# Kernel optimization log

Hardware: AMD Instinct MI355X
Metric: run time of the kernel (lower is better)

Reference implementation:

```python
import jax, jax.numpy as jnp
import numpy as np

B, S, D, H, DFF = 4, 2048, 1024, 16, 4096
DK = D // H
EPS = 1e-5


def _linear_params(key, fan_in, fan_out):
    kw, kb = jax.random.split(key)
    bound = 1.0 / np.sqrt(fan_in)
    w = jax.random.uniform(kw, (fan_in, fan_out), minval=-bound, maxval=bound, dtype=jnp.float32)
    b = jax.random.uniform(kb, (fan_out,), minval=-bound, maxval=bound, dtype=jnp.float32)
    return w, b


def setup_inputs() -> dict:
    key = jax.random.key(0)
    ks = jax.random.split(key, 8)
    x = jax.random.normal(ks[0], (B, S, D), dtype=jnp.float32)
    mask = jnp.ones((B, 1, 1, S), dtype=jnp.int32)
    wq, bq = _linear_params(ks[1], D, D)
    wk, bk = _linear_params(ks[2], D, D)
    wv, bv = _linear_params(ks[3], D, D)
    wo, bo = _linear_params(ks[4], D, D)
    w1, b1 = _linear_params(ks[5], D, DFF)
    w2, b2 = _linear_params(ks[6], DFF, D)
    g1 = jnp.ones((D,), jnp.float32); be1 = jnp.zeros((D,), jnp.float32)
    g2 = jnp.ones((D,), jnp.float32); be2 = jnp.zeros((D,), jnp.float32)
    return {"x": x, "mask": mask, "wq": wq, "bq": bq, "wk": wk, "bk": bk,
            "wv": wv, "bv": bv, "wo": wo, "bo": bo, "w1": w1, "b1": b1,
            "w2": w2, "b2": b2, "g1": g1, "be1": be1, "g2": g2, "be2": be2}


def _layernorm(x, g, b):
    mu = jnp.mean(x, axis=-1, keepdims=True)
    var = jnp.mean(jnp.square(x - mu), axis=-1, keepdims=True)
    return (x - mu) * jax.lax.rsqrt(var + EPS) * g + b


def reference(x, mask, wq, bq, wk, bk, wv, bv, wo, bo, w1, b1, w2, b2, g1, be1, g2, be2):
    # Multi-head self-attention
    q = (x @ wq + bq).reshape(B, S, H, DK).transpose(0, 2, 1, 3)  # b h s d
    k = (x @ wk + bk).reshape(B, S, H, DK).transpose(0, 2, 1, 3)
    v = (x @ wv + bv).reshape(B, S, H, DK).transpose(0, 2, 1, 3)
    scores = jnp.einsum('bhqd,bhkd->bhqk', q, k) / np.sqrt(DK)
    scores = jnp.where(mask == 0, jnp.float32(-1e9), scores)
    attn = jax.nn.softmax(scores, axis=-1)
    ctx = jnp.einsum('bhqk,bhkd->bhqd', attn, v)
    ctx = ctx.transpose(0, 2, 1, 3).reshape(B, S, D)
    attn_out = ctx @ wo + bo
    # Dropout is identity in eval mode
    out1 = _layernorm(x + attn_out, g1, be1)
    ffn = jax.nn.relu(out1 @ w1 + b1) @ w2 + b2
    out2 = _layernorm(out1 + ffn, g2, be2)
    return out2
```

## Files before the change

### kernel.cpp

```cpp
#include <hip/hip_runtime.h>
#include <cstdint>
#include <cstddef>

typedef __bf16 bf16_t;
typedef __bf16 bf16x4 __attribute__((ext_vector_type(4)));
typedef __bf16 bf16x8 __attribute__((ext_vector_type(8)));
typedef float f32x4 __attribute__((ext_vector_type(4)));

#define GLD_LDS16(g, l)                                                                   \
  __builtin_amdgcn_global_load_lds((const __attribute__((address_space(1))) void*)(g),   \
                                   (__attribute__((address_space(3))) void*)(l), 16, 0, 0)

__device__ __forceinline__ int swbits(int row) {
  return ((row ^ (row >> 3)) & 7) << 4;
}
__device__ __forceinline__ int swz(int row, int colbyte) {
  return row * 128 + (colbyte ^ swbits(row));
}

__global__ __launch_bounds__(256) void transpose_cvt_k(const float* __restrict__ src,
                                                       bf16_t* __restrict__ dst, int R, int C) {
  __shared__ float t[64][65];
  const int tid = threadIdx.x;
  const int tr = blockIdx.y * 64, tc = blockIdx.x * 64;
  const int r0 = tid >> 2, c0 = (tid & 3) * 16;
#pragma unroll
  for (int i = 0; i < 16; i += 4) {
    float4 v = *(const float4*)(src + (size_t)(tr + r0) * C + tc + c0 + i);
    t[r0][c0 + i] = v.x; t[r0][c0 + i + 1] = v.y;
    t[r0][c0 + i + 2] = v.z; t[r0][c0 + i + 3] = v.w;
  }
  __syncthreads();
  bf16x8 w0, w1;
#pragma unroll
  for (int i = 0; i < 8; ++i) {
    w0[i] = (bf16_t)t[c0 + i][r0];
    w1[i] = (bf16_t)t[c0 + 8 + i][r0];
  }
  *(bf16x8*)(dst + (size_t)(tc + r0) * R + tr + c0) = w0;
  *(bf16x8*)(dst + (size_t)(tc + r0) * R + tr + c0 + 8) = w1;
}

__global__ __launch_bounds__(256) void cvt_k(const float* __restrict__ in,
                                             bf16_t* __restrict__ out) {
  const size_t i = ((size_t)blockIdx.x * 256 + threadIdx.x) * 8;
  float4 a = *(const float4*)(in + i);
  float4 b = *(const float4*)(in + i + 4);
  bf16x8 o;
  o[0] = (bf16_t)a.x; o[1] = (bf16_t)a.y; o[2] = (bf16_t)a.z; o[3] = (bf16_t)a.w;
  o[4] = (bf16_t)b.x; o[5] = (bf16_t)b.y; o[6] = (bf16_t)b.z; o[7] = (bf16_t)b.w;
  *(bf16x8*)(out + i) = o;
}

__global__ void mask_scan_k(const int* __restrict__ mask, unsigned* __restrict__ dirty) {
  __shared__ int tilez[32];
  const int tid = threadIdx.x;
  for (int b = 0; b < 4; ++b) {
    if (tid < 32) tilez[tid] = 0;
    __syncthreads();
    int anyz = 0;
    const int* mb = mask + b * 2048 + tid * 8;
#pragma unroll
    for (int j = 0; j < 8; ++j) anyz |= (mb[j] == 0);
    if (anyz) atomicOr(&tilez[tid >> 3], 1);
    __syncthreads();
    if (tid == 0) {
      unsigned w = 0;
      for (int k = 0; k < 32; ++k) w |= (tilez[k] ? 1u : 0u) << k;
      dirty[b] = w;
    }
    __syncthreads();
  }
}

template <int EPI>
__global__ __launch_bounds__(512, 1) void gemmA(
    const bf16_t* __restrict__ A, const bf16_t* __restrict__ Bt,
    const float* __restrict__ bias0, const float* __restrict__ bias1,
    const float* __restrict__ bias2, const bf16_t* __restrict__ res,
    bf16_t* __restrict__ out0, bf16_t* __restrict__ out1, bf16_t* __restrict__ out2,
    int N, int K) {
  extern __shared__ __align__(16) char lds[];
  const int tid = threadIdx.x, lane = tid & 63, wave = tid >> 6;
  const int fr = lane & 15, hi = lane >> 4;
  const int wm = wave >> 1, wn = wave & 1;
  const int tile_n = blockIdx.x * 128, tile_m = blockIdx.y * 256;
  const int NT = K >> 6;
  const int s_r = tid >> 3, s_cb = (tid & 7) * 16;

  f32x4 acc[4][4];
#pragma unroll
  for (int m = 0; m < 4; ++m)
#pragma unroll
    for (int n = 0; n < 4; ++n)
#pragma unroll
      for (int c = 0; c < 4; ++c) acc[m][n][c] = 0.f;

#define STAGEA(t, cbuf)                                                                    \
  do {                                                                                     \
    const size_t k0_ = (size_t)(t) * 64;                                                   \
    _Pragma("unroll") for (int i_ = 0; i_ < 4; ++i_) {                                     \
      GLD_LDS16(A + (size_t)(tile_m + i_ * 64 + s_r) * K + k0_ + ((s_cb ^ swbits(s_r)) >> 1),\
                lds + (cbuf)*49152 + i_ * 8192 + wave * 1024);                             \
    }                                                                                      \
    _Pragma("unroll") for (int i_ = 0; i_ < 2; ++i_) {                                     \
      GLD_LDS16(Bt + (size_t)(tile_n + i_ * 64 + s_r) * K + k0_ + ((s_cb ^ swbits(s_r)) >> 1),\
                lds + (cbuf)*49152 + 32768 + i_ * 8192 + wave * 1024);                     \
    }                                                                                      \
  } while (0)

  STAGEA(0, 0);
  for (int t = 0; t < NT; ++t) {
    const int c = t & 1;
    if (t + 1 < NT) {
      STAGEA(t + 1, c ^ 1);
      asm volatile("s_waitcnt vmcnt(6)" ::: "memory");
    } else {
      asm volatile("s_waitcnt vmcnt(0)" ::: "memory");
    }
    __builtin_amdgcn_s_barrier();

    bf16x8 bfrag[4][2];
#pragma unroll
    for (int n = 0; n < 4; ++n)
#pragma unroll
      for (int kk = 0; kk < 2; ++kk)
        bfrag[n][kk] = *(const bf16x8*)(lds + c * 49152 + 32768 + wn * 8192 +
                                        swz(n * 16 + fr, kk * 64 + hi * 16));
    bf16x8 af[2][2][2];
#pragma unroll
    for (int mm = 0; mm < 2; ++mm)
#pragma unroll
      for (int kk = 0; kk < 2; ++kk)
        af[0][mm][kk] = *(const bf16x8*)(lds + c * 49152 + wm * 8192 +
                                         swz(mm * 16 + fr, kk * 64 + hi * 16));
#pragma unroll
    for (int p = 0; p < 2; ++p) {
      if (p < 1) {
#pragma unroll
        for (int mm = 0; mm < 2; ++mm)
#pragma unroll
          for (int kk = 0; kk < 2; ++kk)
            af[1][mm][kk] = *(const bf16x8*)(lds + c * 49152 + wm * 8192 +
                                             swz((2 + mm) * 16 + fr, kk * 64 + hi * 16));
      }
      __builtin_amdgcn_s_setprio(1);
#pragma unroll
      for (int mm = 0; mm < 2; ++mm)
#pragma unroll
        for (int n = 0; n < 4; ++n)
#pragma unroll
          for (int kk = 0; kk < 2; ++kk)
            acc[p * 2 + mm][n] = __builtin_amdgcn_mfma_f32_16x16x32_bf16(
                af[p][mm][kk], bfrag[n][kk], acc[p * 2 + mm][n], 0, 0, 0);
      __builtin_amdgcn_s_setprio(0);
    }
    __builtin_amdgcn_s_barrier();
  }
#undef STAGEA

#pragma unroll
  for (int m = 0; m < 4; ++m) {
#pragma unroll
    for (int n = 0; n < 4; ++n) {
      const int col = tile_n + wn * 64 + n * 16 + fr;
      const int rbase = tile_m + wm * 64 + m * 16 + hi * 4;
      if constexpr (EPI == 0) {
        const int which = tile_n >> 10;
        const float* bp = which == 0 ? bias0 : (which == 1 ? bias1 : bias2);
        bf16_t* op = which == 0 ? out0 : (which == 1 ? out1 : out2);
        const float sca = which == 0 ? 0.18033688f : 1.0f;
        const int cc = col & 1023, h = cc >> 6, dk = cc & 63;
        const float bv = bp[cc];
#pragma unroll
        for (int r = 0; r < 4; ++r) {
          const int row = rbase + r, bb = row >> 11, ss = row & 2047;
          op[(((size_t)bb * 16 + h) * 2048 + ss) * 64 + dk] = (bf16_t)((acc[m][n][r] + bv) * sca);
        }
      } else {
        const float bv = bias0[col];
#pragma unroll
        for (int r = 0; r < 4; ++r) {
          const int row = rbase + r;
          float v = acc[m][n][r] + bv + (float)res[(size_t)row * N + col];
          out0[(size_t)row * N + col] = (bf16_t)v;
        }
      }
    }
  }
}

template <int EPI>
__global__ __launch_bounds__(512, 1) void gemm256(
    const bf16_t* __restrict__ A, const bf16_t* __restrict__ Bt,
    const float* __restrict__ bias0,
    bf16_t* __restrict__ out0, int N, int K) {
  extern __shared__ __align__(16) char lds[];
  const int tid = threadIdx.x, lane = tid & 63, wave = tid >> 6;
  const int fr = lane & 15, hi = lane >> 4;
  const int wm = wave >> 2, wn = wave & 3;
  const int tile_n = blockIdx.x * 256, tile_m = blockIdx.y * 256;
  const int NT = K >> 6;
  const int s_r = tid >> 3, s_cb = (tid & 7) * 16;

  f32x4 acc[8][4];
#pragma unroll
  for (int m = 0; m < 8; ++m)
#pragma unroll
    for (int n = 0; n < 4; ++n)
#pragma unroll
      for (int c = 0; c < 4; ++c) acc[m][n][c] = 0.f;

#define STAGE256(t, cbuf)                                                                  \
  do {                                                                                     \
    const size_t k0_ = (size_t)(t) * 64;                                                   \
    _Pragma("unroll") for (int h_ = 0; h_ < 2; ++h_)                                       \
        _Pragma("unroll") for (int is_ = 0; is_ < 2; ++is_) {                              \
      const int r_ = is_ * 64 + s_r;                                                       \
      GLD_LDS16(A + (size_t)(tile_m + h_ * 128 + r_) * K + k0_ + ((s_cb ^ swbits(r_)) >> 1),\
                lds + (cbuf)*65536 + h_ * 16384 + is_ * 8192 + wave * 1024);               \
    }                                                                                      \
    _Pragma("unroll") for (int h_ = 0; h_ < 2; ++h_)                                       \
        _Pragma("unroll") for (int is_ = 0; is_ < 2; ++is_) {                              \
      const int r_ = is_ * 64 + s_r;                                                       \
      GLD_LDS16(Bt + (size_t)(tile_n + h_ * 128 + r_) * K + k0_ + ((s_cb ^ swbits(r_)) >> 1),\
                lds + (cbuf)*65536 + 32768 + h_ * 16384 + is_ * 8192 + wave * 1024);       \
    }                                                                                      \
  } while (0)

  STAGE256(0, 0);
  for (int t = 0; t < NT; ++t) {
    const int c = t & 1;
    if (t + 1 < NT) {
      STAGE256(t + 1, c ^ 1);
      asm volatile("s_waitcnt vmcnt(8)" ::: "memory");
    } else {
      asm volatile("s_waitcnt vmcnt(0)" ::: "memory");
    }
    __builtin_amdgcn_s_barrier();

    bf16x8 bfrag[4][2];
#pragma unroll
    for (int n = 0; n < 4; ++n)
#pragma unroll
      for (int kk = 0; kk < 2; ++kk)
        bfrag[n][kk] = *(const bf16x8*)(lds + c * 65536 + 32768 + (wn >> 1) * 16384 +
                                        swz((wn & 1) * 64 + n * 16 + fr, kk * 64 + hi * 16));
    bf16x8 af[2][2][2];
#pragma unroll
    for (int mm = 0; mm < 2; ++mm)
#pragma unroll
      for (int kk = 0; kk < 2; ++kk)
        af[0][mm][kk] = *(const bf16x8*)(lds + c * 65536 + wm * 16384 +
                                         swz(mm * 16 + fr, kk * 64 + hi * 16));
#pragma unroll
    for (int p = 0; p < 4; ++p) {
      if (p < 3) {
#pragma unroll
        for (int mm = 0; mm < 2; ++mm)
#pragma unroll
          for (int kk = 0; kk < 2; ++kk)
            af[(p + 1) & 1][mm][kk] =
                *(const bf16x8*)(lds + c * 65536 + wm * 16384 +
                                 swz(((p + 1) * 2 + mm) * 16 + fr, kk * 64 + hi * 16));
      }
      __builtin_amdgcn_s_setprio(1);
#pragma unroll
      for (int mm = 0; mm < 2; ++mm)
#pragma unroll
        for (int n = 0; n < 4; ++n)
#pragma unroll
          for (int kk = 0; kk < 2; ++kk)
            acc[p * 2 + mm][n] = __builtin_amdgcn_mfma_f32_16x16x32_bf16(
                af[p & 1][mm][kk], bfrag[n][kk], acc[p * 2 + mm][n], 0, 0, 0);
      __builtin_amdgcn_s_setprio(0);
    }
    __builtin_amdgcn_s_barrier();
  }
#undef STAGE256

#pragma unroll
  for (int m = 0; m < 8; ++m) {
#pragma unroll
    for (int n = 0; n < 4; ++n) {
      const int col = tile_n + wn * 64 + n * 16 + fr;
      const int rbase = tile_m + wm * 128 + m * 16 + hi * 4;
      const float bv = bias0[col];
#pragma unroll
      for (int r = 0; r < 4; ++r) {
        const int row = rbase + r;
        float v = acc[m][n][r] + bv;
        if constexpr (EPI == 2) v = v > 0.f ? v : 0.f;
        out0[(size_t)row * N + col] = (bf16_t)v;
      }
    }
  }
}

__global__ __launch_bounds__(256) void attn_k(
    const bf16_t* __restrict__ Q, const bf16_t* __restrict__ Kb, const bf16_t* __restrict__ Vb,
    const int* __restrict__ mask, const unsigned* __restrict__ dirtyp,
    bf16_t* __restrict__ ctxout) {
  __shared__ __align__(16) char Qs[16384];
  __shared__ __align__(16) char Ks[2][8192];
  __shared__ __align__(16) char Vt[2][8192];
  __shared__ __align__(16) char Ps[16384];
  const int tid = threadIdx.x, lane = tid & 63, wave = tid >> 6;
  const int fr = lane & 15, hi = lane >> 4;
  const int qt = blockIdx.x, bh = blockIdx.y, b = bh >> 4, h = bh & 15;
  const bf16_t* qbase = Q + ((size_t)bh * 2048 + qt * 128) * 64;
  const bf16_t* kbase = Kb + (size_t)bh * 2048 * 64;
  const bf16_t* vbase = Vb + (size_t)bh * 2048 * 64;
  const int* mbase = mask + b * 2048;
  const unsigned dirty = dirtyp[b];

  const int src_r = tid >> 3;
  const int src_cb = (tid & 7) * 16;

#pragma unroll
  for (int j = 0; j < 4; ++j) {
    const int c = j * 256 + tid, rr = c >> 3, cb = (c & 7) * 16;
    GLD_LDS16(qbase + rr * 64 + ((cb ^ swbits(rr)) >> 1), Qs + j * 4096 + wave * 1024);
  }
#pragma unroll
  for (int j = 0; j < 2; ++j) {
    const int rr = j * 32 + src_r;
    GLD_LDS16(kbase + rr * 64 + ((src_cb ^ swbits(rr)) >> 1), Ks[0] + j * 4096 + wave * 1024);
  }
  {
    bf16x8 v0 = *(const bf16x8*)(vbase + (size_t)(tid >> 3) * 64 + (tid & 7) * 8);
    bf16x8 v1 = *(const bf16x8*)(vbase + (size_t)(32 + (tid >> 3)) * 64 + (tid & 7) * 8);
    const int kp0 = tid >> 3, kp1 = 32 + (tid >> 3), d0 = (tid & 7) * 8;
#pragma unroll
    for (int i = 0; i < 8; ++i) {
      *(bf16_t*)(Vt[0] + swz(d0 + i, kp0 * 2)) = v0[i];
      *(bf16_t*)(Vt[0] + swz(d0 + i, kp1 * 2)) = v1[i];
    }
  }
  __syncthreads();

  f32x4 ctx[2][4];
  float l_prt[2][4];
#pragma unroll
  for (int mi = 0; mi < 2; ++mi)
#pragma unroll
    for (int r = 0; r < 4; ++r) {
      l_prt[mi][r] = 0.f;
#pragma unroll
      for (int di = 0; di < 4; ++di) ctx[mi][di][r] = 0.f;
    }

  for (int kt = 0; kt < 32; ++kt) {
    const int cur = kt & 1;
    bf16x8 vr0, vr1;
    if (kt < 31) {
#pragma unroll
      for (int j = 0; j < 2; ++j) {
        const int rr = j * 32 + src_r;
        GLD_LDS16(kbase + (size_t)(kt + 1) * 4096 + rr * 64 + ((src_cb ^ swbits(rr)) >> 1),
                  Ks[cur ^ 1] + j * 4096 + wave * 1024);
      }
      vr0 = *(const bf16x8*)(vbase + (size_t)(kt + 1) * 4096 + (size_t)(tid >> 3) * 64 +
                             (tid & 7) * 8);
      vr1 = *(const bf16x8*)(vbase + (size_t)(kt + 1) * 4096 + (size_t)(32 + (tid >> 3)) * 64 +
                             (tid & 7) * 8);
    }

    f32x4 sc[2][4];
#pragma unroll
    for (int mi = 0; mi < 2; ++mi)
#pragma unroll
      for (int ni = 0; ni < 4; ++ni)
#pragma unroll
        for (int c = 0; c < 4; ++c) sc[mi][ni][c] = 0.f;
#pragma unroll
    for (int kk = 0; kk < 2; ++kk) {
      bf16x8 aq[2], kb_[4];
#pragma unroll
      for (int mi = 0; mi < 2; ++mi)
        aq[mi] = *(const bf16x8*)(Qs + swz(wave * 32 + mi * 16 + fr, kk * 64 + hi * 16));
#pragma unroll
      for (int ni = 0; ni < 4; ++ni)
        kb_[ni] = *(const bf16x8*)(Ks[cur] + swz(ni * 16 + fr, kk * 64 + hi * 16));
#pragma unroll
      for (int mi = 0; mi < 2; ++mi)
#pragma unroll
        for (int ni = 0; ni < 4; ++ni)
          sc[mi][ni] = __builtin_amdgcn_mfma_f32_16x16x32_bf16(aq[mi], kb_[ni], sc[mi][ni], 0, 0, 0);
    }

    if (dirty & (1u << kt)) {
      int mv[4];
#pragma unroll
      for (int ni = 0; ni < 4; ++ni) mv[ni] = mbase[kt * 64 + ni * 16 + fr];
#pragma unroll
      for (int mi = 0; mi < 2; ++mi)
#pragma unroll
        for (int ni = 0; ni < 4; ++ni)
#pragma unroll
          for (int r = 0; r < 4; ++r)
            sc[mi][ni][r] = mv[ni] ? sc[mi][ni][r] : -1e9f;
    }

#pragma unroll
    for (int mi = 0; mi < 2; ++mi) {
#pragma unroll
      for (int r = 0; r < 4; ++r) {
        float rsum = 0.f;
#pragma unroll
        for (int ni = 0; ni < 4; ++ni) {
          const float p = exp2f(sc[mi][ni][r]);
          sc[mi][ni][r] = p;
          rsum += p;
        }
        l_prt[mi][r] += rsum;
      }
      const int qrow = wave * 32 + mi * 16 + hi * 4;
#pragma unroll
      for (int ni = 0; ni < 4; ++ni)
#pragma unroll
        for (int r = 0; r < 4; ++r)
          *(bf16_t*)(Ps + swz(qrow + r, (ni * 16 + fr) * 2)) = (bf16_t)sc[mi][ni][r];
    }
    asm volatile("s_waitcnt lgkmcnt(0)" ::: "memory");
    __builtin_amdgcn_sched_barrier(0);

#pragma unroll
    for (int kk = 0; kk < 2; ++kk) {
      bf16x8 pa[2], vv[4];
#pragma unroll
      for (int mi = 0; mi < 2; ++mi)
        pa[mi] = *(const bf16x8*)(Ps + swz(wave * 32 + mi * 16 + fr, kk * 64 + hi * 16));
#pragma unroll
      for (int di = 0; di < 4; ++di)
        vv[di] = *(const bf16x8*)(Vt[cur] + swz(di * 16 + fr, kk * 64 + hi * 16));
#pragma unroll
      for (int mi = 0; mi < 2; ++mi)
#pragma unroll
        for (int di = 0; di < 4; ++di)
          ctx[mi][di] =
              __builtin_amdgcn_mfma_f32_16x16x32_bf16(pa[mi], vv[di], ctx[mi][di], 0, 0, 0);
    }

    if (kt < 31) {
      const int kp0 = tid >> 3, kp1 = 32 + (tid >> 3), d0 = (tid & 7) * 8;
#pragma unroll
      for (int i = 0; i < 8; ++i) {
        *(bf16_t*)(Vt[cur ^ 1] + swz(d0 + i, kp0 * 2)) = vr0[i];
        *(bf16_t*)(Vt[cur ^ 1] + swz(d0 + i, kp1 * 2)) = vr1[i];
      }
    }
    __syncthreads();
  }

#pragma unroll
  for (int mi = 0; mi < 2; ++mi)
#pragma unroll
    for (int r = 0; r < 4; ++r) {
      float l = l_prt[mi][r];
#pragma unroll
      for (int d = 1; d < 16; d <<= 1) l += __shfl_xor(l, d);
      const float inv = 1.f / l;
      const int srow = qt * 128 + wave * 32 + mi * 16 + hi * 4 + r;
#pragma unroll
      for (int di = 0; di < 4; ++di) {
        const int col = h * 64 + di * 16 + fr;
        ctxout[((size_t)b * 2048 + srow) * 1024 + col] = (bf16_t)(ctx[mi][di][r] * inv);
      }
    }
}

template <int F32OUT>
__global__ __launch_bounds__(256) void ln_k(const bf16_t* __restrict__ in,
                                            const float* __restrict__ g,
                                            const float* __restrict__ be,
                                            void* __restrict__ out) {
  __shared__ float red[8];
  const int tid = threadIdx.x;
  const size_t row = blockIdx.x;
  bf16x4 v4 = *(const bf16x4*)(in + row * 1024 + tid * 4);
  const float f0 = (float)v4[0], f1 = (float)v4[1], f2 = (float)v4[2], f3 = (float)v4[3];
  float s = f0 + f1 + f2 + f3;
  float s2 = f0 * f0 + f1 * f1 + f2 * f2 + f3 * f3;
#pragma unroll
  for (int d = 1; d < 64; d <<= 1) { s += __shfl_xor(s, d); s2 += __shfl_xor(s2, d); }
  if ((tid & 63) == 0) { red[tid >> 6] = s; red[4 + (tid >> 6)] = s2; }
  __syncthreads();
  s = red[0] + red[1] + red[2] + red[3];
  s2 = red[4] + red[5] + red[6] + red[7];
  const float mu = s * (1.f / 1024.f);
  const float var = s2 * (1.f / 1024.f) - mu * mu;
  const float rs = rsqrtf(var + 1e-5f);
  float4 gv = *(const float4*)(g + tid * 4);
  float4 bv = *(const float4*)(be + tid * 4);
  const float r0 = (f0 - mu) * rs * gv.x + bv.x;
  const float r1 = (f1 - mu) * rs * gv.y + bv.y;
  const float r2 = (f2 - mu) * rs * gv.z + bv.z;
  const float r3 = (f3 - mu) * rs * gv.w + bv.w;
  if constexpr (F32OUT) {
    float4 o = {r0, r1, r2, r3};
    *(float4*)((float*)out + row * 1024 + tid * 4) = o;
  } else {
    bf16x4 o;
    o[0] = (bf16_t)r0; o[1] = (bf16_t)r1; o[2] = (bf16_t)r2; o[3] = (bf16_t)r3;
    *(bf16x4*)((bf16_t*)out + row * 1024 + tid * 4) = o;
  }
}

extern "C" void kernel_launch(void* const* d_in, const int* in_sizes, int n_in,
                              void* d_out, int out_size, void* d_ws, size_t ws_size,
                              hipStream_t stream) {
  const float* x    = (const float*)d_in[0];
  const int*   mask = (const int*)d_in[1];
  const float* wq = (const float*)d_in[2];
  const float* bq = (const float*)d_in[3];
  const float* wk = (const float*)d_in[4];
  const float* bk = (const float*)d_in[5];
  const float* wv = (const float*)d_in[6];
  const float* bv = (const float*)d_in[7];
  const float* wo = (const float*)d_in[8];
  const float* bo = (const float*)d_in[9];
  const float* w1 = (const float*)d_in[10];
  const float* b1 = (const float*)d_in[11];
  const float* w2 = (const float*)d_in[12];
  const float* b2 = (const float*)d_in[13];
  const float* g1  = (const float*)d_in[14];
  const float* be1 = (const float*)d_in[15];
  const float* g2  = (const float*)d_in[16];
  const float* be2 = (const float*)d_in[17];

  char* wsb = (char*)d_ws;
  bf16_t* S0  = (bf16_t*)wsb;
  bf16_t* XB  = (bf16_t*)(wsb + 8388608);
  bf16_t* QB  = (bf16_t*)(wsb + 25165824);
  bf16_t* KB  = (bf16_t*)(wsb + 41943040);
  bf16_t* VB  = (bf16_t*)(wsb + 58720256);
  bf16_t* CTX = (bf16_t*)(wsb + 75497472);
  bf16_t* FFN = QB;
  bf16_t* Y   = (bf16_t*)(wsb + 92274688);
  bf16_t* O1  = (bf16_t*)(wsb + 109051904);
  unsigned* DIRTY = (unsigned*)(wsb + 125829120);

  (void)hipFuncSetAttribute((const void*)gemmA<0>,
                            hipFuncAttributeMaxDynamicSharedMemorySize, 98304);
  (void)hipFuncSetAttribute((const void*)gemmA<1>,
                            hipFuncAttributeMaxDynamicSharedMemorySize, 98304);
  (void)hipFuncSetAttribute((const void*)gemm256<2>,
                            hipFuncAttributeMaxDynamicSharedMemorySize, 131072);

  dim3 blk(256);
  mask_scan_k<<<1, 256, 0, stream>>>(mask, DIRTY);
  cvt_k<<<4096, blk, 0, stream>>>(x, XB);
  transpose_cvt_k<<<dim3(16, 16), blk, 0, stream>>>(wq, S0, 1024, 1024);
  transpose_cvt_k<<<dim3(16, 16), blk, 0, stream>>>(wk, S0 + 1048576, 1024, 1024);
  transpose_cvt_k<<<dim3(16, 16), blk, 0, stream>>>(wv, S0 + 2097152, 1024, 1024);
  gemmA<0><<<dim3(24, 32), 512, 98304, stream>>>(XB, S0, bq, bk, bv, nullptr,
                                                 QB, KB, VB, 3072, 1024);
  transpose_cvt_k<<<dim3(16, 16), blk, 0, stream>>>(wo, S0, 1024, 1024);
  attn_k<<<dim3(16, 64), blk, 0, stream>>>(QB, KB, VB, mask, DIRTY, CTX);
  gemmA<1><<<dim3(8, 32), 512, 98304, stream>>>(CTX, S0, bo, nullptr, nullptr, XB,
                                                Y, nullptr, nullptr, 1024, 1024);
  transpose_cvt_k<<<dim3(64, 16), blk, 0, stream>>>(w1, S0, 1024, 4096);
  ln_k<0><<<8192, blk, 0, stream>>>(Y, g1, be1, O1);
  gemm256<2><<<dim3(16, 32), 512, 131072, stream>>>(O1, S0, b1, FFN, 4096, 1024);
  transpose_cvt_k<<<dim3(16, 64), blk, 0, stream>>>(w2, S0, 4096, 1024);
  gemmA<1><<<dim3(8, 32), 512, 98304, stream>>>(FFN, S0, b2, nullptr, nullptr, O1,
                                                Y, nullptr, nullptr, 1024, 4096);
  ln_k<1><<<8192, blk, 0, stream>>>(Y, g2, be2, d_out);
}
```

Before: 467.7 us.

## Batch QKV weight transposes, remap attention blocks per XCD, raise MFMA priority

Merges the three QKV weight transpose launches into one 3D-grid kernel. The attention block index is remapped so that consecutive query tiles of the same head land on the same XCD, which should improve L2 reuse of K/V. s_setprio is raised around the MFMA bursts in attention. Together these target launch overhead, cache locality and wave scheduling. The remap assumes a fixed grid of 1024 blocks and eight XCDs.

New measurement: 466.1 us. Within noise of the previous version (-0.3%).

```diff
diff --git a/kernel.cpp b/kernel.cpp
--- a/kernel.cpp
+++ b/kernel.cpp
@@ -39,6 +39,33 @@
   }
   *(bf16x8*)(dst + (size_t)(tc + r0) * R + tr + c0) = w0;
   *(bf16x8*)(dst + (size_t)(tc + r0) * R + tr + c0 + 8) = w1;
+}
+
+__global__ __launch_bounds__(256) void transpose3_cvt_k(const float* __restrict__ s0,
+                                                        const float* __restrict__ s1,
+                                                        const float* __restrict__ s2,
+                                                        bf16_t* __restrict__ dst) {
+  __shared__ float t[64][65];
+  const int tid = threadIdx.x, z = blockIdx.z;
+  const float* src = z == 0 ? s0 : (z == 1 ? s1 : s2);
+  bf16_t* d = dst + (size_t)z * 1048576;
+  const int tr = blockIdx.y * 64, tc = blockIdx.x * 64;
+  const int r0 = tid >> 2, c0 = (tid & 3) * 16;
+#pragma unroll
+  for (int i = 0; i < 16; i += 4) {
+    float4 v = *(const float4*)(src + (size_t)(tr + r0) * 1024 + tc + c0 + i);
+    t[r0][c0 + i] = v.x; t[r0][c0 + i + 1] = v.y;
+    t[r0][c0 + i + 2] = v.z; t[r0][c0 + i + 3] = v.w;
+  }
+  __syncthreads();
+  bf16x8 w0, w1;
+#pragma unroll
+  for (int i = 0; i < 8; ++i) {
+    w0[i] = (bf16_t)t[c0 + i][r0];
+    w1[i] = (bf16_t)t[c0 + 8 + i][r0];
+  }
+  *(bf16x8*)(d + (size_t)(tc + r0) * 1024 + tr + c0) = w0;
+  *(bf16x8*)(d + (size_t)(tc + r0) * 1024 + tr + c0 + 8) = w1;
 }
 
 __global__ __launch_bounds__(256) void cvt_k(const float* __restrict__ in,
@@ -307,7 +334,9 @@
   __shared__ __align__(16) char Ps[16384];
   const int tid = threadIdx.x, lane = tid & 63, wave = tid >> 6;
   const int fr = lane & 15, hi = lane >> 4;
-  const int qt = blockIdx.x, bh = blockIdx.y, b = bh >> 4, h = bh & 15;
+  const int hw = blockIdx.x + (blockIdx.y << 4);
+  const int wid = (hw & 7) * 128 + (hw >> 3);
+  const int qt = wid & 15, bh = wid >> 4, b = bh >> 4, h = bh & 15;
   const bf16_t* qbase = Q + ((size_t)bh * 2048 + qt * 128) * 64;
   const bf16_t* kbase = Kb + (size_t)bh * 2048 * 64;
   const bf16_t* vbase = Vb + (size_t)bh * 2048 * 64;
@@ -382,11 +411,13 @@
 #pragma unroll
       for (int ni = 0; ni < 4; ++ni)
         kb_[ni] = *(const bf16x8*)(Ks[cur] + swz(ni * 16 + fr, kk * 64 + hi * 16));
+      __builtin_amdgcn_s_setprio(1);
 #pragma unroll
       for (int mi = 0; mi < 2; ++mi)
 #pragma unroll
         for (int ni = 0; ni < 4; ++ni)
           sc[mi][ni] = __builtin_amdgcn_mfma_f32_16x16x32_bf16(aq[mi], kb_[ni], sc[mi][ni], 0, 0, 0);
+      __builtin_amdgcn_s_setprio(0);
     }
 
     if (dirty & (1u << kt)) {
@@ -434,12 +465,14 @@
 #pragma unroll
       for (int di = 0; di < 4; ++di)
         vv[di] = *(const bf16x8*)(Vt[cur] + swz(di * 16 + fr, kk * 64 + hi * 16));
+      __builtin_amdgcn_s_setprio(1);
 #pragma unroll
       for (int mi = 0; mi < 2; ++mi)
 #pragma unroll
         for (int di = 0; di < 4; ++di)
           ctx[mi][di] =
               __builtin_amdgcn_mfma_f32_16x16x32_bf16(pa[mi], vv[di], ctx[mi][di], 0, 0, 0);
+      __builtin_amdgcn_s_setprio(0);
     }
 
     if (kt < 31) {
@@ -551,9 +584,7 @@
   dim3 blk(256);
   mask_scan_k<<<1, 256, 0, stream>>>(mask, DIRTY);
   cvt_k<<<4096, blk, 0, stream>>>(x, XB);
-  transpose_cvt_k<<<dim3(16, 16), blk, 0, stream>>>(wq, S0, 1024, 1024);
-  transpose_cvt_k<<<dim3(16, 16), blk, 0, stream>>>(wk, S0 + 1048576, 1024, 1024);
-  transpose_cvt_k<<<dim3(16, 16), blk, 0, stream>>>(wv, S0 + 2097152, 1024, 1024);
+  transpose3_cvt_k<<<dim3(16, 16, 3), blk, 0, stream>>>(wq, wk, wv, S0);
   gemmA<0><<<dim3(24, 32), 512, 98304, stream>>>(XB, S0, bq, bk, bv, nullptr,
                                                  QB, KB, VB, 3072, 1024);
   transpose_cvt_k<<<dim3(16, 16), blk, 0, stream>>>(wo, S0, 1024, 1024);
```
